# Kernel optimization log

Hardware: AMD Instinct MI355X
Metric: run time of the kernel (lower is better)

The kernel has to match this reference:

```python
import jax, jax.numpy as jnp
import numpy as np

IN_DIMS = 256
EMBED_DIMS = 512
NUM_HEADS = 8
GRID = 16  # forced: arrange2 hardcodes 256 = GRID*GRID tokens
HEAD_DIM = EMBED_DIMS // NUM_HEADS
LN_EPS = 1e-5


def setup_inputs() -> dict:
    key = jax.random.key(0)
    ks = jax.random.split(key, 12)
    B = 8
    s_in = 1.0 / np.sqrt(IN_DIMS)
    s_emb = 1.0 / np.sqrt(EMBED_DIMS)
    return {
        "x1": jax.random.normal(ks[0], (B, IN_DIMS, GRID, GRID), jnp.float32),
        "x2": jax.random.normal(ks[1], (B, IN_DIMS, GRID, GRID), jnp.float32),
        # 1x1 conv weights stored as [out, in]
        "Wq": jax.random.normal(ks[2], (EMBED_DIMS, IN_DIMS), jnp.float32) * s_in,
        "bq": jnp.zeros((EMBED_DIMS,), jnp.float32),
        "Wk": jax.random.normal(ks[3], (EMBED_DIMS, IN_DIMS), jnp.float32) * s_in,
        "bk": jnp.zeros((EMBED_DIMS,), jnp.float32),
        "Wv": jax.random.normal(ks[4], (EMBED_DIMS, IN_DIMS), jnp.float32) * s_in,
        "bv": jnp.zeros((EMBED_DIMS,), jnp.float32),
        "Wa": jax.random.normal(ks[5], (IN_DIMS, EMBED_DIMS), jnp.float32) * s_emb,
        "ba": jnp.zeros((IN_DIMS,), jnp.float32),
        "ln_g": jnp.ones((IN_DIMS,), jnp.float32),
        "ln_b": jnp.zeros((IN_DIMS,), jnp.float32),
        "Wl": jax.random.normal(ks[6], (IN_DIMS, IN_DIMS), jnp.float32) * s_in,
        "bl": jnp.zeros((IN_DIMS,), jnp.float32),
    }


def _conv1x1(x, W, b):
    # x: [b, Cin, h, w]; W: [Cout, Cin]
    return jnp.einsum('bihw,oi->bohw', x, W) + b[None, :, None, None]


def _arrange(t):
    # 'b (c head) h w -> head b (h w) c'  (c outer, head inner in channel axis)
    b = t.shape[0]
    t = t.reshape(b, HEAD_DIM, NUM_HEADS, GRID * GRID)
    return t.transpose(2, 0, 3, 1)  # [head, b, n, c]


def reference(x1, x2, Wq, bq, Wk, bk, Wv, bv, Wa, ba, ln_g, ln_b, Wl, bl):
    B, Cin, H, W = x1.shape
    N = H * W  # 256
    q = _arrange(_conv1x1(x1, Wq, bq))                     # [h, b, n, c]
    k = _arrange(_conv1x1(x2, Wk, bk))                     # [h, q, m, c]
    v = _arrange(_conv1x1(x2, Wv, bv)).reshape(NUM_HEADS, B * N, HEAD_DIM)  # [h, (b m), c]
    # cross-batch attention logits (NOTE: original never applies self.scale)
    attn = jnp.einsum('pbnc,pqmc->pbqnm', q, k)            # [h, b, q, n, m]
    attn = jax.nn.softmax(attn, axis=-1)
    # 'head b q n m -> b head n (q m)'
    attn = attn.transpose(1, 0, 3, 2, 4).reshape(B, NUM_HEADS, N, B * N)
    out = jnp.einsum('bhnm,hmc->bhnc', attn, v)            # [b, h, n, c]
    # 'b head (h w) c -> b (c head) h w'
    out = out.transpose(0, 3, 1, 2).reshape(B, EMBED_DIMS, H, W)
    a = _conv1x1(out, Wa, ba) + x1                          # residual, [b, Cin, h, w]
    # proj_out: rearrange -> LayerNorm -> Linear -> ReLU -> rearrange back
    t = a.reshape(B, Cin, N).transpose(0, 2, 1)            # [b, n, Cin]
    mu = t.mean(-1, keepdims=True)
    var = ((t - mu) ** 2).mean(-1, keepdims=True)
    t = (t - mu) * jax.lax.rsqrt(var + LN_EPS) * ln_g + ln_b
    t = jax.nn.relu(t @ Wl.T + bl)
    return t.transpose(0, 2, 1).reshape(B, Cin, H, W)
```

## Files before the change

### kernel.cpp

```cpp
#include <hip/hip_runtime.h>

typedef unsigned short u16;
typedef unsigned int   u32;
typedef __attribute__((ext_vector_type(8))) short bf16x8;
typedef __attribute__((ext_vector_type(4))) float f32x4;

#define BB   8
#define CIN  256
#define NT   256
#define EMB  512
#define NH   8

__device__ __forceinline__ float bf2f(u16 b) {
    union { u32 u; float f; } v; v.u = ((u32)b) << 16; return v.f;
}
__device__ __forceinline__ u16 f2bf(float f) {
    union { float f; u32 u; } v; v.f = f;
    u32 r = v.u + 0x7FFFu + ((v.u >> 16) & 1u);
    return (u16)(r >> 16);
}
__device__ __forceinline__ float ld(const u16* base, size_t idx, int f32) {
    return f32 ? ((const float*)base)[idx] : bf2f(base[idx]);
}

struct alignas(16) U32x4 { u32 x, y, z, w; };

#define FMA44(AP, S, A4, B4) do { \
  (AP)[0*(S)+0] += (A4).x*(B4).x; (AP)[0*(S)+1] += (A4).x*(B4).y; (AP)[0*(S)+2] += (A4).x*(B4).z; (AP)[0*(S)+3] += (A4).x*(B4).w; \
  (AP)[1*(S)+0] += (A4).y*(B4).x; (AP)[1*(S)+1] += (A4).y*(B4).y; (AP)[1*(S)+2] += (A4).y*(B4).z; (AP)[1*(S)+3] += (A4).y*(B4).w; \
  (AP)[2*(S)+0] += (A4).z*(B4).x; (AP)[2*(S)+1] += (A4).z*(B4).y; (AP)[2*(S)+2] += (A4).z*(B4).z; (AP)[2*(S)+3] += (A4).z*(B4).w; \
  (AP)[3*(S)+0] += (A4).w*(B4).x; (AP)[3*(S)+1] += (A4).w*(B4).y; (AP)[3*(S)+2] += (A4).w*(B4).z; (AP)[3*(S)+3] += (A4).w*(B4).w; \
} while (0)

__global__ void k_detect(const u16* __restrict__ x1, int* __restrict__ flag) {
    __shared__ int cnt;
    if (threadIdx.x == 0) cnt = 0;
    __syncthreads();
    int t = threadIdx.x;
    int local = 0;
    for (int j = t * 16; j < t * 16 + 16; j += 2) {
        u16 w = x1[j];
        int e = (w >> 7) & 0xFF;
        if (e >= 100 && e <= 145) local++;
    }
    atomicAdd(&cnt, local);
    __syncthreads();
    if (t == 0) *flag = (cnt >= 1200) ? 0 : 1;
}

__global__ void k_xpose(
    const u16* __restrict__ x1, const u16* __restrict__ x2,
    const u16* __restrict__ Wq, const u16* __restrict__ Wk, const u16* __restrict__ Wv,
    u16* __restrict__ XTh, u16* __restrict__ XTl,
    u16* __restrict__ WCh, u16* __restrict__ WCl)
{
    __shared__ int cnt;
    __shared__ float T[64][65];
    int t = threadIdx.x;
    if (t == 0) cnt = 0;
    __syncthreads();
    {
        int local = 0;
        for (int j = t * 16; j < t * 16 + 16; j += 2) {
            u16 w = x1[j];
            int e = (w >> 7) & 0xFF;
            if (e >= 100 && e <= 145) local++;
        }
        atomicAdd(&cnt, local);
    }
    __syncthreads();
    const int f32 = (cnt >= 1200) ? 0 : 1;

    int bid = blockIdx.x;
    if (bid < 256) {
        int inp = bid >> 7, b = (bid >> 4) & 7, ks = (bid >> 2) & 3, ns = bid & 3;
        const u16* X = inp ? x2 : x1;
#pragma unroll
        for (int p = 0; p < 4; ++p) {
            int kk = p * 16 + (t >> 4);
            int nn = (t & 15) * 4;
#pragma unroll
            for (int j = 0; j < 4; ++j)
                T[kk][nn + j] = ld(X, ((size_t)b * CIN + ks * 64 + kk) * NT + ns * 64 + nn + j, f32);
        }
        __syncthreads();
#pragma unroll
        for (int it = 0; it < 2; ++it) {
            int g = it * 256 + t;
            int nn = g >> 3, kg = g & 7;
            u32 hw[4], lw[4];
#pragma unroll
            for (int e = 0; e < 4; ++e) {
                float va = T[kg * 8 + 2 * e][nn];
                float vb = T[kg * 8 + 2 * e + 1][nn];
                u16 ha = f2bf(va), hb = f2bf(vb);
                u16 la = f2bf(va - bf2f(ha)), lb = f2bf(vb - bf2f(hb));
                hw[e] = (u32)ha | ((u32)hb << 16);
                lw[e] = (u32)la | ((u32)lb << 16);
            }
            size_t dst = (((size_t)(inp * 8 + b) * 256) + ns * 64 + nn) * 256 + ks * 64 + kg * 8;
            U32x4 H; H.x = hw[0]; H.y = hw[1]; H.z = hw[2]; H.w = hw[3];
            U32x4 L; L.x = lw[0]; L.y = lw[1]; L.z = lw[2]; L.w = lw[3];
            *(U32x4*)&XTh[dst] = H;
            *(U32x4*)&XTl[dst] = L;
        }
    } else {
        int wb = bid - 256;
        int proj = wb >> 2, qtr = wb & 3;
        const u16* W = (proj == 0) ? Wq : (proj == 1) ? Wk : Wv;
#pragma unroll
        for (int it = 0; it < 16; ++it) {
            int g = it * 256 + t;
            int row = g >> 5, kg = g & 31;
            int o = qtr * 128 + row;
            u32 hw[4], lw[4];
#pragma unroll
            for (int e = 0; e < 4; ++e) {
                float va = ld(W, (size_t)o * CIN + kg * 8 + 2 * e, f32);
                float vb = ld(W, (size_t)o * CIN + kg * 8 + 2 * e + 1, f32);
                u16 ha = f2bf(va), hb = f2bf(vb);
                u16 la = f2bf(va - bf2f(ha)), lb = f2bf(vb - bf2f(hb));
                hw[e] = (u32)ha | ((u32)hb << 16);
                lw[e] = (u32)la | ((u32)lb << 16);
            }
            size_t dst = ((size_t)(proj * 512 + o)) * 256 + kg * 8;
            U32x4 H; H.x = hw[0]; H.y = hw[1]; H.z = hw[2]; H.w = hw[3];
            U32x4 L; L.x = lw[0]; L.y = lw[1]; L.z = lw[2]; L.w = lw[3];
            *(U32x4*)&WCh[dst] = H;
            *(U32x4*)&WCl[dst] = L;
        }
    }
}

__global__ __launch_bounds__(256) void k_qkv(
    const u16* __restrict__ XTh, const u16* __restrict__ XTl,
    const u16* __restrict__ WCh, const u16* __restrict__ WCl,
    const u16* __restrict__ bq, const u16* __restrict__ bk, const u16* __restrict__ bv,
    u16* __restrict__ Qg, u16* __restrict__ Kg, u16* __restrict__ Vg,
    const int* __restrict__ flag)
{
    const int f32 = *flag;
    int id = blockIdx.x;
    int proj = id >> 8;
    int rem  = id & 255;
    int b  = rem >> 5;
    int ot = (rem >> 2) & 7;
    int nt = rem & 3;

    __shared__ __align__(16) u16 SB[16384];
    const int WHO = 0, WLO = 4096, XHO = 8192, XLO = 12288;

    int t = threadIdx.x;
    int l = t & 63, w = t >> 6;
    int quad = l >> 4, col = l & 15;
    const int lswz2 = l ^ (((l >> 4) & 1) << 1);

    const u16* Wh  = WCh + ((size_t)proj * 512 + ot * 64) * 256;
    const u16* Wlo = WCl + ((size_t)proj * 512 + ot * 64) * 256;
    int inp = (proj == 0) ? 0 : 1;
    const u16* Xh  = XTh + (((size_t)(inp * 8 + b)) * 256 + nt * 64) * 256;
    const u16* Xlo = XTl + (((size_t)(inp * 8 + b)) * 256 + nt * 64) * 256;

    f32x4 acc[4];
#pragma unroll
    for (int n4 = 0; n4 < 4; ++n4) { acc[n4][0]=0.f; acc[n4][1]=0.f; acc[n4][2]=0.f; acc[n4][3]=0.f; }

    for (int c4 = 0; c4 < 4; ++c4) {
        __syncthreads();
#pragma unroll
        for (int it = 0; it < 2; ++it) {
            int g = it * 256 + t;
            int row = g >> 3, cc = g & 7;
            int tt = row >> 4, klo = row & 15, kch = cc >> 2, qs = cc & 3;
            int pos = qs * 16 + (klo ^ ((qs & 1) << 1) ^ (kch << 2));
            int off = ((tt * 2 + kch) * 64 + pos) * 8;
            size_t src = (size_t)row * 256 + c4 * 64 + cc * 8;
            *(U32x4*)&SB[WHO + off] = *(const U32x4*)&Wh[src];
            *(U32x4*)&SB[WLO + off] = *(const U32x4*)&Wlo[src];
            *(U32x4*)&SB[XHO + off] = *(const U32x4*)&Xh[src];
            *(U32x4*)&SB[XLO + off] = *(const U32x4*)&Xlo[src];
        }
        __syncthreads();

        int sA0 = ((w * 2 + 0) * 64 + lswz2) * 8;
        int sA1 = ((w * 2 + 1) * 64 + (lswz2 ^ 4)) * 8;
        bf16x8 aH0 = *(const bf16x8*)&SB[WHO + sA0];
        bf16x8 aH1 = *(const bf16x8*)&SB[WHO + sA1];
        bf16x8 aL0 = *(const bf16x8*)&SB[WLO + sA0];
        bf16x8 aL1 = *(const bf16x8*)&SB[WLO + sA1];
#pragma unroll
        for (int n4 = 0; n4 < 4; ++n4) {
            int sB0 = ((n4 * 2 + 0) * 64 + lswz2) * 8;
            int sB1 = ((n4 * 2 + 1) * 64 + (lswz2 ^ 4)) * 8;
            bf16x8 bH0 = *(const bf16x8*)&SB[XHO + sB0];
            bf16x8 bH1 = *(const bf16x8*)&SB[XHO + sB1];
            bf16x8 bL0 = *(const bf16x8*)&SB[XLO + sB0];
            bf16x8 bL1 = *(const bf16x8*)&SB[XLO + sB1];
            acc[n4] = __builtin_amdgcn_mfma_f32_16x16x32_bf16(aH0, bH0, acc[n4], 0, 0, 0);
            acc[n4] = __builtin_amdgcn_mfma_f32_16x16x32_bf16(aH1, bH1, acc[n4], 0, 0, 0);
            acc[n4] = __builtin_amdgcn_mfma_f32_16x16x32_bf16(aL0, bH0, acc[n4], 0, 0, 0);
            acc[n4] = __builtin_amdgcn_mfma_f32_16x16x32_bf16(aL1, bH1, acc[n4], 0, 0, 0);
            acc[n4] = __builtin_amdgcn_mfma_f32_16x16x32_bf16(aH0, bL0, acc[n4], 0, 0, 0);
            acc[n4] = __builtin_amdgcn_mfma_f32_16x16x32_bf16(aH1, bL1, acc[n4], 0, 0, 0);
        }
    }
    __syncthreads();

    float (*EP)[68] = (float (*)[68])SB;
    const u16* bias = (proj == 0) ? bq : (proj == 1) ? bk : bv;
#pragma unroll
    for (int r = 0; r < 4; ++r) {
        int ol = w * 16 + quad * 4 + r;
        float bb = ld(bias, ot * 64 + ol, f32);
#pragma unroll
        for (int n4 = 0; n4 < 4; ++n4)
            EP[ol][n4 * 16 + col] = acc[n4][r] + bb;
    }
    __syncthreads();

    if (proj < 2) {
        u16* OUT = (proj == 0) ? Qg : Kg;
        int hh = t >> 5;
        int nb = t & 31;
#pragma unroll
        for (int p = 0; p < 2; ++p) {
            int nn = nb + 32 * p;
            u32 pk[4];
#pragma unroll
            for (int e = 0; e < 4; ++e) {
                u16 lo = f2bf(EP[(2 * e) * 8 + hh][nn]);
                u16 hi = f2bf(EP[(2 * e + 1) * 8 + hh][nn]);
                pk[e] = (u32)lo | ((u32)hi << 16);
            }
            U32x4 v; v.x = pk[0]; v.y = pk[1]; v.z = pk[2]; v.w = pk[3];
            *(U32x4*)&OUT[((size_t)((hh * 8 + b) * 256) + nt * 64 + nn) * 64 + ot * 8] = v;
        }
    } else {
        int rr = t >> 2;
        int hh = rr & 7, cl = rr >> 3;
        int nq = t & 3;
        u32 pk[8];
#pragma unroll
        for (int e = 0; e < 8; ++e) {
            u16 lo = f2bf(EP[cl * 8 + hh][nq * 16 + 2 * e]);
            u16 hi = f2bf(EP[cl * 8 + hh][nq * 16 + 2 * e + 1]);
            pk[e] = (u32)lo | ((u32)hi << 16);
        }
        size_t base = ((size_t)((hh * 8 + b) * 64) + ot * 8 + cl) * 256 + nt * 64 + nq * 16;
        U32x4 v0; v0.x = pk[0]; v0.y = pk[1]; v0.z = pk[2]; v0.w = pk[3];
        U32x4 v1; v1.x = pk[4]; v1.y = pk[5]; v1.z = pk[6]; v1.w = pk[7];
        *(U32x4*)&Vg[base]     = v0;
        *(U32x4*)&Vg[base + 8] = v1;
    }
}

__global__ __launch_bounds__(256) void k_attn(
    const u16* __restrict__ Qg, const u16* __restrict__ Kg,
    const u16* __restrict__ Vg, float* __restrict__ Oph)
{
    int bid = blockIdx.x;
    int h   = bid >> 6;
    int kbg = (bid >> 5) & 1;
    int b   = (bid >> 2) & 7;
    int ntq = bid & 3;

    int t = threadIdx.x;
    int l = t & 63, w = t >> 6;
    int quad = l >> 4, col = l & 15;

    __shared__ __align__(16) u16 S[16384];

    int q = ntq*64 + w*16 + col;
    const size_t qrow = ((size_t)(h*8 + b)*256 + q)*64;
    bf16x8 qf0 = *(const bf16x8*)&Qg[qrow +  0 + quad*8];
    bf16x8 qf1 = *(const bf16x8*)&Qg[qrow + 32 + quad*8];

    const int lswz2 = l ^ (((l >> 4) & 1) << 1);
    const int lswz4 = l ^ (((l >> 4) & 1) << 2);

    f32x4 Oacc[4];
#pragma unroll
    for (int ct = 0; ct < 4; ++ct) { Oacc[ct][0]=0.f; Oacc[ct][1]=0.f; Oacc[ct][2]=0.f; Oacc[ct][3]=0.f; }

    for (int kb2 = 0; kb2 < 4; ++kb2) {
        int kb = kbg*4 + kb2;
        __syncthreads();
        const size_t kbase = (size_t)(h*8 + kb) * 256 * 64;
#pragma unroll
        for (int i = 0; i < 8; ++i) {
            int g = i*256 + t;
            int key = g >> 3, cc = g & 7;
            int tt = key >> 4, klo = key & 15, kc = cc >> 2, qs = cc & 3;
            int pos = qs*16 + (klo ^ ((qs & 1) << 1) ^ (kc << 2));
            U32x4 v = *(const U32x4*)&Kg[kbase + (size_t)key*64 + cc*8];
            *(U32x4*)&S[(size_t)(((tt*2 + kc)*64) + pos)*8] = v;
        }
        __syncthreads();

        f32x4 Sfr[16];
#pragma unroll
        for (int tt = 0; tt < 16; ++tt) { Sfr[tt][0]=0.f; Sfr[tt][1]=0.f; Sfr[tt][2]=0.f; Sfr[tt][3]=0.f; }
#pragma unroll
        for (int tt = 0; tt < 16; ++tt) {
            bf16x8 k0 = *(const bf16x8*)&S[(size_t)((tt*2 + 0)*64 + lswz2)*8];
            bf16x8 k1 = *(const bf16x8*)&S[(size_t)((tt*2 + 1)*64 + (lswz2 ^ 4))*8];
            Sfr[tt] = __builtin_amdgcn_mfma_f32_16x16x32_bf16(k0, qf0, Sfr[tt], 0, 0, 0);
            Sfr[tt] = __builtin_amdgcn_mfma_f32_16x16x32_bf16(k1, qf1, Sfr[tt], 0, 0, 0);
        }

        float inv;
        {
            float m = Sfr[0][0];
#pragma unroll
            for (int tt = 0; tt < 16; ++tt)
#pragma unroll
                for (int r = 0; r < 4; ++r) m = fmaxf(m, Sfr[tt][r]);
            m = fmaxf(m, __shfl_xor(m, 16));
            m = fmaxf(m, __shfl_xor(m, 32));
            float s = 0.f;
#pragma unroll
            for (int tt = 0; tt < 16; ++tt)
#pragma unroll
                for (int r = 0; r < 4; ++r) {
                    float e = __expf(Sfr[tt][r] - m);
                    Sfr[tt][r] = e; s += e;
                }
            s += __shfl_xor(s, 16);
            s += __shfl_xor(s, 32);
            inv = 1.f / s;
        }

        bf16x8 pf[8];
#pragma unroll
        for (int ch = 0; ch < 8; ++ch) {
            float a0 = Sfr[2*ch  ][0]*inv, a1 = Sfr[2*ch  ][1]*inv;
            float a2 = Sfr[2*ch  ][2]*inv, a3 = Sfr[2*ch  ][3]*inv;
            float b0 = Sfr[2*ch+1][0]*inv, b1 = Sfr[2*ch+1][1]*inv;
            float b2 = Sfr[2*ch+1][2]*inv, b3 = Sfr[2*ch+1][3]*inv;
            u32 u0, u1, v0, v1;
            asm("v_cvt_pk_bf16_f32 %0, %1, %2" : "=v"(u0) : "v"(a0), "v"(a1));
            asm("v_cvt_pk_bf16_f32 %0, %1, %2" : "=v"(u1) : "v"(a2), "v"(a3));
            asm("v_cvt_pk_bf16_f32 %0, %1, %2" : "=v"(v0) : "v"(b0), "v"(b1));
            asm("v_cvt_pk_bf16_f32 %0, %1, %2" : "=v"(v1) : "v"(b2), "v"(b3));
            asm("v_permlane32_swap_b32 %0, %1" : "+v"(u0), "+v"(v0));
            asm("v_permlane16_swap_b32 %0, %1" : "+v"(u0), "+v"(v0));
            asm("v_permlane32_swap_b32 %0, %1" : "+v"(u1), "+v"(v1));
            asm("v_permlane16_swap_b32 %0, %1" : "+v"(u1), "+v"(v1));
            union { u32 wd[4]; bf16x8 hB; } pu;
            pu.wd[0] = u0; pu.wd[1] = u1; pu.wd[2] = v0; pu.wd[3] = v1;
            pf[ch] = pu.hB;
        }
        __syncthreads();

        const size_t vbase = (size_t)(h*8 + kb) * 64 * 256;
#pragma unroll
        for (int i = 0; i < 8; ++i) {
            int g = i*256 + t;
            int cg = g >> 5, k16 = g & 31;
            int ct = cg >> 4, clo = cg & 15, ch = k16 >> 2, qs = k16 & 3;
            int pos = (qs*16 + clo) ^ ch ^ ((qs & 1) << 2);
            U32x4 v = *(const U32x4*)&Vg[vbase + (size_t)cg*256 + k16*8];
            *(U32x4*)&S[(size_t)(((ch*4 + ct)*64) + pos)*8] = v;
        }
        __syncthreads();

#pragma unroll
        for (int ch = 0; ch < 8; ++ch)
#pragma unroll
            for (int ct = 0; ct < 4; ++ct) {
                bf16x8 vb = *(const bf16x8*)&S[(size_t)(((ch*4 + ct)*64) + (lswz4 ^ ch))*8];
                Oacc[ct] = __builtin_amdgcn_mfma_f32_16x16x32_bf16(pf[ch], vb, Oacc[ct], 0, 0, 0);
            }
    }

    float* Op = Oph + (size_t)kbg * ((size_t)BB * EMB * NT);
    const size_t obase = (size_t)(h*8 + b) * 256 * 64;
    int n0 = ntq*64 + w*16 + quad*4;
#pragma unroll
    for (int ct = 0; ct < 4; ++ct)
#pragma unroll
        for (int r = 0; r < 4; ++r)
            Op[obase + (size_t)(n0 + r)*64 + ct*16 + col] = Oacc[ct][r];
}

__global__ void k_proj_res(
    const float* __restrict__ Oph, const u16* __restrict__ Wa,
    const u16* __restrict__ ba, const u16* __restrict__ x1,
    float* __restrict__ Ap, const int* __restrict__ flag)
{
    const int f32 = *flag;
    int id = blockIdx.x;
    int tt = id >> 2;
    int it = id & 3;
    int tok0 = tt * 32;
    int b  = tok0 >> 8;
    int n0 = tok0 & 255;

    __shared__ float Was[64][68];
    __shared__ float Os[64][36];

    int t = threadIdx.x;
    int lane64 = t & 63, quad = t >> 6;
    int ig = t & 15;
    int tg = t >> 4;

    int tk = t & 31;
    int hh = t >> 5;

    const size_t SLAB = (size_t)BB * EMB * NT;

    float wreg[16];
    float oreg[8];

    {
#pragma unroll
        for (int p = 0; p < 16; ++p) {
            int i = quad + 4*p;
            wreg[p] = ld(Wa, (size_t)(it*64 + i)*EMB + 0*64 + lane64, f32);
        }
        const float* src = &Oph[(((size_t)(hh*8 + b))*256 + n0 + tk)*64 + 0*8];
        float4 v0 = *(const float4*)&src[0];
        float4 v1 = *(const float4*)&src[4];
        float4 u0 = *(const float4*)&src[SLAB];
        float4 u1 = *(const float4*)&src[SLAB + 4];
        oreg[0]=v0.x+u0.x; oreg[1]=v0.y+u0.y; oreg[2]=v0.z+u0.z; oreg[3]=v0.w+u0.w;
        oreg[4]=v1.x+u1.x; oreg[5]=v1.y+u1.y; oreg[6]=v1.z+u1.z; oreg[7]=v1.w+u1.w;
    }

    float acc[8];
#pragma unroll
    for (int j = 0; j < 8; ++j) acc[j] = 0.f;

    for (int kc = 0; kc < 8; ++kc) {
        __syncthreads();
#pragma unroll
        for (int p = 0; p < 16; ++p)
            Was[lane64][quad + 4*p] = wreg[p];
#pragma unroll
        for (int e = 0; e < 8; ++e)
            Os[e*8 + hh][tk] = oreg[e];
        __syncthreads();

        if (kc < 7) {
            int kn = kc + 1;
#pragma unroll
            for (int p = 0; p < 16; ++p) {
                int i = quad + 4*p;
                wreg[p] = ld(Wa, (size_t)(it*64 + i)*EMB + kn*64 + lane64, f32);
            }
            const float* src = &Oph[(((size_t)(hh*8 + b))*256 + n0 + tk)*64 + kn*8];
            float4 v0 = *(const float4*)&src[0];
            float4 v1 = *(const float4*)&src[4];
            float4 u0 = *(const float4*)&src[SLAB];
            float4 u1 = *(const float4*)&src[SLAB + 4];
            oreg[0]=v0.x+u0.x; oreg[1]=v0.y+u0.y; oreg[2]=v0.z+u0.z; oreg[3]=v0.w+u0.w;
            oreg[4]=v1.x+u1.x; oreg[5]=v1.y+u1.y; oreg[6]=v1.z+u1.z; oreg[7]=v1.w+u1.w;
        }

#pragma unroll 8
        for (int o = 0; o < 64; ++o) {
            float4 w4 = *(const float4*)&Was[o][ig*4];
            float2 t2 = *(const float2*)&Os[o][tg*2];
            acc[0] += w4.x*t2.x; acc[1] += w4.y*t2.x;
            acc[2] += w4.z*t2.x; acc[3] += w4.w*t2.x;
            acc[4] += w4.x*t2.y; acc[5] += w4.y*t2.y;
            acc[6] += w4.z*t2.y; acc[7] += w4.w*t2.y;
        }
    }

    int i0 = it*64 + ig*4;
    float ba0 = ld(ba, i0+0, f32), ba1 = ld(ba, i0+1, f32);
    float ba2 = ld(ba, i0+2, f32), ba3 = ld(ba, i0+3, f32);
#pragma unroll
    for (int jt = 0; jt < 2; ++jt) {
        int token = tok0 + tg*2 + jt;
        int n = n0 + tg*2 + jt;
        float4 v;
        v.x = acc[jt*4+0] + ba0 + ld(x1, ((size_t)b*CIN + i0+0)*NT + n, f32);
        v.y = acc[jt*4+1] + ba1 + ld(x1, ((size_t)b*CIN + i0+1)*NT + n, f32);
        v.z = acc[jt*4+2] + ba2 + ld(x1, ((size_t)b*CIN + i0+2)*NT + n, f32);
        v.w = acc[jt*4+3] + ba3 + ld(x1, ((size_t)b*CIN + i0+3)*NT + n, f32);
        *(float4*)&Ap[(size_t)token*CIN + i0] = v;
    }
}

__global__ void k_ln_out(
    const float* __restrict__ Ap, const u16* __restrict__ ln_g,
    const u16* __restrict__ ln_b, const u16* __restrict__ Wl,
    const u16* __restrict__ bl, u16* __restrict__ out,
    const int* __restrict__ flag)
{
    const int f32 = *flag;
    int tok0 = blockIdx.x * 8;
    int b  = tok0 >> 8;
    int n0 = tok0 & 255;

    __shared__ float At[8][260];

    int t = threadIdx.x;
#pragma unroll
    for (int k = 0; k < 8; ++k)
        At[k][t] = Ap[((size_t)tok0 + k)*CIN + t];
    __syncthreads();

    {
        int kk = t >> 5, lme = t & 31;
        float s = 0.f, s2 = 0.f;
#pragma unroll
        for (int ii = 0; ii < 8; ++ii) { float v = At[kk][lme + 32*ii]; s += v; s2 += v*v; }
#pragma unroll
        for (int off = 1; off < 32; off <<= 1) { s += __shfl_xor(s, off); s2 += __shfl_xor(s2, off); }
        float mu   = s  * (1.f/256.f);
        float var  = s2 * (1.f/256.f) - mu*mu;
        float rstd = rsqrtf(var + 1e-5f);
#pragma unroll
        for (int ii = 0; ii < 8; ++ii) {
            int i = lme + 32*ii;
            float v = At[kk][i];
            At[kk][i] = (v - mu) * rstd * ld(ln_g, i, f32) + ld(ln_b, i, f32);
        }
    }
    __syncthreads();

    int j = t;
    float acc[8];
#pragma unroll
    for (int k = 0; k < 8; ++k) acc[k] = 0.f;

    if (f32) {
        const float* wrow = (const float*)Wl + (size_t)j*CIN;
#pragma unroll 2
        for (int i4 = 0; i4 < 64; ++i4) {
            float4 w4 = *(const float4*)&wrow[4*i4];
#pragma unroll
            for (int k = 0; k < 8; ++k) {
                float4 a = *(const float4*)&At[k][4*i4];
                acc[k] += w4.x*a.x + w4.y*a.y + w4.z*a.z + w4.w*a.w;
            }
        }
    } else {
        const u32* wrow = (const u32*)(Wl + (size_t)j*CIN);
#pragma unroll 2
        for (int i4 = 0; i4 < 64; ++i4) {
            u32 w01 = wrow[2*i4+0], w23 = wrow[2*i4+1];
            float c0 = bf2f((u16)(w01 & 0xFFFFu)), c1 = bf2f((u16)(w01 >> 16));
            float c2 = bf2f((u16)(w23 & 0xFFFFu)), c3 = bf2f((u16)(w23 >> 16));
#pragma unroll
            for (int k = 0; k < 8; ++k) {
                float4 a = *(const float4*)&At[k][4*i4];
                acc[k] += c0*a.x + c1*a.y + c2*a.z + c3*a.w;
            }
        }
    }

    float blv = ld(bl, j, f32);
    size_t obase = ((size_t)b*CIN + j)*NT + n0;
    if (f32) {
        float* o32 = (float*)out;
#pragma unroll
        for (int k = 0; k < 8; ++k)
            o32[obase + k] = fmaxf(acc[k] + blv, 0.f);
    } else {
        u32 pk[4];
#pragma unroll
        for (int k = 0; k < 4; ++k) {
            float f0 = fmaxf(acc[2*k+0] + blv, 0.f);
            float f1 = fmaxf(acc[2*k+1] + blv, 0.f);
            pk[k] = (u32)f2bf(f0) | ((u32)f2bf(f1) << 16);
        }
        U32x4 a0; a0.x = pk[0]; a0.y = pk[1]; a0.z = pk[2]; a0.w = pk[3];
        *(U32x4*)(out + obase) = a0;
    }
}

extern "C" void kernel_launch(void* const* d_in, const int* in_sizes, int n_in,
                              void* d_out, int out_size, void* d_ws, size_t ws_size,
                              hipStream_t stream)
{
    const u16* x1   = (const u16*)d_in[0];
    const u16* x2   = (const u16*)d_in[1];
    const u16* Wq   = (const u16*)d_in[2];
    const u16* bq   = (const u16*)d_in[3];
    const u16* Wk   = (const u16*)d_in[4];
    const u16* bk   = (const u16*)d_in[5];
    const u16* Wv   = (const u16*)d_in[6];
    const u16* bv   = (const u16*)d_in[7];
    const u16* Wa   = (const u16*)d_in[8];
    const u16* ba   = (const u16*)d_in[9];
    const u16* ln_g = (const u16*)d_in[10];
    const u16* ln_b = (const u16*)d_in[11];
    const u16* Wl   = (const u16*)d_in[12];
    const u16* bl   = (const u16*)d_in[13];
    u16* out = (u16*)d_out;

    int* flag = (int*)d_ws;
    u16* Qg = (u16*)d_ws + 32;
    u16* Kg = Qg + (size_t)BB*EMB*NT;
    u16* Vg = Kg + (size_t)BB*EMB*NT;
    float* Oph = (float*)(Vg + (size_t)BB*EMB*NT);
    float* Ap  = Oph + 2*(size_t)BB*EMB*NT;
    u16* XTh = (u16*)(Ap + (size_t)BB*NT*CIN);
    u16* XTl = XTh + (size_t)2*BB*NT*CIN;
    u16* WCh = XTl + (size_t)2*BB*NT*CIN;
    u16* WCl = WCh + (size_t)3*EMB*CIN;

    k_detect  <<<1,   256, 0, stream>>>(x1, flag);
    k_xpose   <<<268, 256, 0, stream>>>(x1, x2, Wq, Wk, Wv, XTh, XTl, WCh, WCl);
    k_qkv     <<<768, 256, 0, stream>>>(XTh, XTl, WCh, WCl, bq, bk, bv, Qg, Kg, Vg, flag);
    k_attn    <<<512, 256, 0, stream>>>(Qg, Kg, Vg, Oph);
    k_proj_res<<<256, 256, 0, stream>>>(Oph, Wa, ba, x1, Ap, flag);
    k_ln_out  <<<256, 256, 0, stream>>>(Ap, ln_g, ln_b, Wl, bl, out, flag);
}
```

Baseline: 185.0 us.

## Split attention key range four ways, fold detect kernel into transpose, reorder grids

The attention kernel now splits the 8 key batches into four groups of two instead of two groups of four, which doubles the grid to 1024 blocks and the number of partial output slabs to four. The projection kernel sums all four slabs. The separate dtype-detect launch is removed and its flag is written by block 0 of the transpose kernel. Block index mappings are reordered so heads and column tiles are interleaved across consecutive blocks. The aim is more parallelism in attention and one less kernel launch, at the cost of more partial-sum traffic and workspace.

Result: no change. 188.3 us (+1.8%).

```diff
diff --git a/kernel.cpp b/kernel.cpp
--- a/kernel.cpp
+++ b/kernel.cpp
@@ -24,35 +24,14 @@
 }
 
 struct alignas(16) U32x4 { u32 x, y, z, w; };
-
-#define FMA44(AP, S, A4, B4) do { \
-  (AP)[0*(S)+0] += (A4).x*(B4).x; (AP)[0*(S)+1] += (A4).x*(B4).y; (AP)[0*(S)+2] += (A4).x*(B4).z; (AP)[0*(S)+3] += (A4).x*(B4).w; \
-  (AP)[1*(S)+0] += (A4).y*(B4).x; (AP)[1*(S)+1] += (A4).y*(B4).y; (AP)[1*(S)+2] += (A4).y*(B4).z; (AP)[1*(S)+3] += (A4).y*(B4).w; \
-  (AP)[2*(S)+0] += (A4).z*(B4).x; (AP)[2*(S)+1] += (A4).z*(B4).y; (AP)[2*(S)+2] += (A4).z*(B4).z; (AP)[2*(S)+3] += (A4).z*(B4).w; \
-  (AP)[3*(S)+0] += (A4).w*(B4).x; (AP)[3*(S)+1] += (A4).w*(B4).y; (AP)[3*(S)+2] += (A4).w*(B4).z; (AP)[3*(S)+3] += (A4).w*(B4).w; \
-} while (0)
-
-__global__ void k_detect(const u16* __restrict__ x1, int* __restrict__ flag) {
-    __shared__ int cnt;
-    if (threadIdx.x == 0) cnt = 0;
-    __syncthreads();
-    int t = threadIdx.x;
-    int local = 0;
-    for (int j = t * 16; j < t * 16 + 16; j += 2) {
-        u16 w = x1[j];
-        int e = (w >> 7) & 0xFF;
-        if (e >= 100 && e <= 145) local++;
-    }
-    atomicAdd(&cnt, local);
-    __syncthreads();
-    if (t == 0) *flag = (cnt >= 1200) ? 0 : 1;
-}
+struct alignas(8)  U32x2 { u32 x, y; };
 
 __global__ void k_xpose(
     const u16* __restrict__ x1, const u16* __restrict__ x2,
     const u16* __restrict__ Wq, const u16* __restrict__ Wk, const u16* __restrict__ Wv,
     u16* __restrict__ XTh, u16* __restrict__ XTl,
-    u16* __restrict__ WCh, u16* __restrict__ WCl)
+    u16* __restrict__ WCh, u16* __restrict__ WCl,
+    int* __restrict__ flag)
 {
     __shared__ int cnt;
     __shared__ float T[64][65];
@@ -72,6 +51,8 @@
     const int f32 = (cnt >= 1200) ? 0 : 1;
 
     int bid = blockIdx.x;
+    if (bid == 0 && t == 0) *flag = f32;
+
     if (bid < 256) {
         int inp = bid >> 7, b = (bid >> 4) & 7, ks = (bid >> 2) & 3, ns = bid & 3;
         const u16* X = inp ? x2 : x1;
@@ -254,15 +235,60 @@
     }
 }
 
+__device__ __forceinline__ void softmax_p(f32x4 (&Sfr)[16], bf16x8 (&pf)[8]) {
+    float inv;
+    {
+        float m = Sfr[0][0];
+#pragma unroll
+        for (int tt = 0; tt < 16; ++tt)
+#pragma unroll
+            for (int r = 0; r < 4; ++r) m = fmaxf(m, Sfr[tt][r]);
+        m = fmaxf(m, __shfl_xor(m, 16));
+        m = fmaxf(m, __shfl_xor(m, 32));
+        float s = 0.f;
+#pragma unroll
+        for (int tt = 0; tt < 16; ++tt)
+#pragma unroll
+            for (int r = 0; r < 4; ++r) {
+                float e = __expf(Sfr[tt][r] - m);
+                Sfr[tt][r] = e; s += e;
+            }
+        s += __shfl_xor(s, 16);
+        s += __shfl_xor(s, 32);
+        inv = 1.f / s;
+    }
+#pragma unroll
+    for (int ch = 0; ch < 8; ++ch) {
+        float a0 = Sfr[2*ch  ][0]*inv, a1 = Sfr[2*ch  ][1]*inv;
+        float a2 = Sfr[2*ch  ][2]*inv, a3 = Sfr[2*ch  ][3]*inv;
+        float b0 = Sfr[2*ch+1][0]*inv, b1 = Sfr[2*ch+1][1]*inv;
+        float b2 = Sfr[2*ch+1][2]*inv, b3 = Sfr[2*ch+1][3]*inv;
+        u32 u0, u1, v0, v1;
+        asm("v_cvt_pk_bf16_f32 %0, %1, %2" : "=v"(u0) : "v"(a0), "v"(a1));
+        asm("v_cvt_pk_bf16_f32 %0, %1, %2" : "=v"(u1) : "v"(a2), "v"(a3));
+        asm("v_cvt_pk_bf16_f32 %0, %1, %2" : "=v"(v0) : "v"(b0), "v"(b1));
+        asm("v_cvt_pk_bf16_f32 %0, %1, %2" : "=v"(v1) : "v"(b2), "v"(b3));
+        asm("v_permlane32_swap_b32 %0, %1" : "+v"(u0), "+v"(v0));
+        asm("v_permlane16_swap_b32 %0, %1" : "+v"(u0), "+v"(v0));
+        asm("v_permlane32_swap_b32 %0, %1" : "+v"(u1), "+v"(v1));
+        asm("v_permlane16_swap_b32 %0, %1" : "+v"(u1), "+v"(v1));
+        union { u32 wd[4]; bf16x8 hB; } pu;
+        pu.wd[0] = u0; pu.wd[1] = u1; pu.wd[2] = v0; pu.wd[3] = v1;
+        pf[ch] = pu.hB;
+    }
+}
+
 __global__ __launch_bounds__(256) void k_attn(
     const u16* __restrict__ Qg, const u16* __restrict__ Kg,
     const u16* __restrict__ Vg, float* __restrict__ Oph)
 {
     int bid = blockIdx.x;
-    int h   = bid >> 6;
-    int kbg = (bid >> 5) & 1;
-    int b   = (bid >> 2) & 7;
-    int ntq = bid & 3;
+    int h      = bid & 7;
+    int slot   = bid >> 3;
+    int kbg    = slot >> 5;
+    int member = slot & 31;
+    int b      = member >> 2;
+    int ntq    = member & 3;
 
     int t = threadIdx.x;
     int l = t & 63, w = t >> 6;
@@ -282,8 +308,8 @@
 #pragma unroll
     for (int ct = 0; ct < 4; ++ct) { Oacc[ct][0]=0.f; Oacc[ct][1]=0.f; Oacc[ct][2]=0.f; Oacc[ct][3]=0.f; }
 
-    for (int kb2 = 0; kb2 < 4; ++kb2) {
-        int kb = kbg*4 + kb2;
+    for (int kb2 = 0; kb2 < 2; ++kb2) {
+        int kb = kbg*2 + kb2;
         __syncthreads();
         const size_t kbase = (size_t)(h*8 + kb) * 256 * 64;
 #pragma unroll
@@ -308,48 +334,8 @@
             Sfr[tt] = __builtin_amdgcn_mfma_f32_16x16x32_bf16(k1, qf1, Sfr[tt], 0, 0, 0);
         }
 
-        float inv;
-        {
-            float m = Sfr[0][0];
-#pragma unroll
-            for (int tt = 0; tt < 16; ++tt)
-#pragma unroll
-                for (int r = 0; r < 4; ++r) m = fmaxf(m, Sfr[tt][r]);
-            m = fmaxf(m, __shfl_xor(m, 16));
-            m = fmaxf(m, __shfl_xor(m, 32));
-            float s = 0.f;
-#pragma unroll
-            for (int tt = 0; tt < 16; ++tt)
-#pragma unroll
-                for (int r = 0; r < 4; ++r) {
-                    float e = __expf(Sfr[tt][r] - m);
-                    Sfr[tt][r] = e; s += e;
-                }
-            s += __shfl_xor(s, 16);
-            s += __shfl_xor(s, 32);
-            inv = 1.f / s;
-        }
-
         bf16x8 pf[8];
-#pragma unroll
-        for (int ch = 0; ch < 8; ++ch) {
-            float a0 = Sfr[2*ch  ][0]*inv, a1 = Sfr[2*ch  ][1]*inv;
-            float a2 = Sfr[2*ch  ][2]*inv, a3 = Sfr[2*ch  ][3]*inv;
-            float b0 = Sfr[2*ch+1][0]*inv, b1 = Sfr[2*ch+1][1]*inv;
-            float b2 = Sfr[2*ch+1][2]*inv, b3 = Sfr[2*ch+1][3]*inv;
-            u32 u0, u1, v0, v1;
-            asm("v_cvt_pk_bf16_f32 %0, %1, %2" : "=v"(u0) : "v"(a0), "v"(a1));
-            asm("v_cvt_pk_bf16_f32 %0, %1, %2" : "=v"(u1) : "v"(a2), "v"(a3));
-            asm("v_cvt_pk_bf16_f32 %0, %1, %2" : "=v"(v0) : "v"(b0), "v"(b1));
-            asm("v_cvt_pk_bf16_f32 %0, %1, %2" : "=v"(v1) : "v"(b2), "v"(b3));
-            asm("v_permlane32_swap_b32 %0, %1" : "+v"(u0), "+v"(v0));
-            asm("v_permlane16_swap_b32 %0, %1" : "+v"(u0), "+v"(v0));
-            asm("v_permlane32_swap_b32 %0, %1" : "+v"(u1), "+v"(v1));
-            asm("v_permlane16_swap_b32 %0, %1" : "+v"(u1), "+v"(v1));
-            union { u32 wd[4]; bf16x8 hB; } pu;
-            pu.wd[0] = u0; pu.wd[1] = u1; pu.wd[2] = v0; pu.wd[3] = v1;
-            pf[ch] = pu.hB;
-        }
+        softmax_p(Sfr, pf);
         __syncthreads();
 
         const size_t vbase = (size_t)(h*8 + kb) * 64 * 256;
@@ -383,15 +369,15 @@
             Op[obase + (size_t)(n0 + r)*64 + ct*16 + col] = Oacc[ct][r];
 }
 
-__global__ void k_proj_res(
+__global__ __launch_bounds__(256) void k_proj_res(
     const float* __restrict__ Oph, const u16* __restrict__ Wa,
     const u16* __restrict__ ba, const u16* __restrict__ x1,
     float* __restrict__ Ap, const int* __restrict__ flag)
 {
     const int f32 = *flag;
     int id = blockIdx.x;
-    int tt = id >> 2;
-    int it = id & 3;
+    int it = id >> 6;
+    int tt = id & 63;
     int tok0 = tt * 32;
     int b  = tok0 >> 8;
     int n0 = tok0 & 255;
@@ -419,12 +405,19 @@
             wreg[p] = ld(Wa, (size_t)(it*64 + i)*EMB + 0*64 + lane64, f32);
         }
         const float* src = &Oph[(((size_t)(hh*8 + b))*256 + n0 + tk)*64 + 0*8];
-        float4 v0 = *(const float4*)&src[0];
-        float4 v1 = *(const float4*)&src[4];
-        float4 u0 = *(const float4*)&src[SLAB];
-        float4 u1 = *(const float4*)&src[SLAB + 4];
-        oreg[0]=v0.x+u0.x; oreg[1]=v0.y+u0.y; oreg[2]=v0.z+u0.z; oreg[3]=v0.w+u0.w;
-        oreg[4]=v1.x+u1.x; oreg[5]=v1.y+u1.y; oreg[6]=v1.z+u1.z; oreg[7]=v1.w+u1.w;
+#pragma unroll
+        for (int s_ = 0; s_ < 4; ++s_) {
+            const float* sp = src + (size_t)s_*SLAB;
+            float4 v0 = *(const float4*)&sp[0];
+            float4 v1 = *(const float4*)&sp[4];
+            if (s_ == 0) {
+                oreg[0]=v0.x; oreg[1]=v0.y; oreg[2]=v0.z; oreg[3]=v0.w;
+                oreg[4]=v1.x; oreg[5]=v1.y; oreg[6]=v1.z; oreg[7]=v1.w;
+            } else {
+                oreg[0]+=v0.x; oreg[1]+=v0.y; oreg[2]+=v0.z; oreg[3]+=v0.w;
+                oreg[4]+=v1.x; oreg[5]+=v1.y; oreg[6]+=v1.z; oreg[7]+=v1.w;
+            }
+        }
     }
 
     float acc[8];
@@ -449,12 +442,19 @@
                 wreg[p] = ld(Wa, (size_t)(it*64 + i)*EMB + kn*64 + lane64, f32);
             }
             const float* src = &Oph[(((size_t)(hh*8 + b))*256 + n0 + tk)*64 + kn*8];
-            float4 v0 = *(const float4*)&src[0];
-            float4 v1 = *(const float4*)&src[4];
-            float4 u0 = *(const float4*)&src[SLAB];
-            float4 u1 = *(const float4*)&src[SLAB + 4];
-            oreg[0]=v0.x+u0.x; oreg[1]=v0.y+u0.y; oreg[2]=v0.z+u0.z; oreg[3]=v0.w+u0.w;
-            oreg[4]=v1.x+u1.x; oreg[5]=v1.y+u1.y; oreg[6]=v1.z+u1.z; oreg[7]=v1.w+u1.w;
+#pragma unroll
+            for (int s_ = 0; s_ < 4; ++s_) {
+                const float* sp = src + (size_t)s_*SLAB;
+                float4 v0 = *(const float4*)&sp[0];
+                float4 v1 = *(const float4*)&sp[4];
+                if (s_ == 0) {
+                    oreg[0]=v0.x; oreg[1]=v0.y; oreg[2]=v0.z; oreg[3]=v0.w;
+                    oreg[4]=v1.x; oreg[5]=v1.y; oreg[6]=v1.z; oreg[7]=v1.w;
+                } else {
+                    oreg[0]+=v0.x; oreg[1]+=v0.y; oreg[2]+=v0.z; oreg[3]+=v0.w;
+                    oreg[4]+=v1.x; oreg[5]+=v1.y; oreg[6]+=v1.z; oreg[7]+=v1.w;
+                }
+            }
         }
 
 #pragma unroll 8
@@ -598,16 +598,15 @@
     u16* Kg = Qg + (size_t)BB*EMB*NT;
     u16* Vg = Kg + (size_t)BB*EMB*NT;
     float* Oph = (float*)(Vg + (size_t)BB*EMB*NT);
-    float* Ap  = Oph + 2*(size_t)BB*EMB*NT;
+    float* Ap  = Oph + 4*(size_t)BB*EMB*NT;
     u16* XTh = (u16*)(Ap + (size_t)BB*NT*CIN);
     u16* XTl = XTh + (size_t)2*BB*NT*CIN;
     u16* WCh = XTl + (size_t)2*BB*NT*CIN;
     u16* WCl = WCh + (size_t)3*EMB*CIN;
 
-    k_detect  <<<1,   256, 0, stream>>>(x1, flag);
-    k_xpose   <<<268, 256, 0, stream>>>(x1, x2, Wq, Wk, Wv, XTh, XTl, WCh, WCl);
-    k_qkv     <<<768, 256, 0, stream>>>(XTh, XTl, WCh, WCl, bq, bk, bv, Qg, Kg, Vg, flag);
-    k_attn    <<<512, 256, 0, stream>>>(Qg, Kg, Vg, Oph);
-    k_proj_res<<<256, 256, 0, stream>>>(Oph, Wa, ba, x1, Ap, flag);
-    k_ln_out  <<<256, 256, 0, stream>>>(Ap, ln_g, ln_b, Wl, bl, out, flag);
-}
+    k_xpose   <<<268,  256, 0, stream>>>(x1, x2, Wq, Wk, Wv, XTh, XTl, WCh, WCl, flag);
+    k_qkv     <<<768,  256, 0, stream>>>(XTh, XTl, WCh, WCl, bq, bk, bv, Qg, Kg, Vg, flag);
+    k_attn    <<<1024, 256, 0, stream>>>(Qg, Kg, Vg, Oph);
+    k_proj_res<<<256,  256, 0, stream>>>(Oph, Wa, ba, x1, Ap, flag);
+    k_ln_out  <<<256,  256, 0, stream>>>(Ap, ln_g, ln_b, Wl, bl, out, flag);
+}
```
